# Kernel optimization log

Hardware: AMD Instinct MI355X
Metric: run time of the kernel (lower is better)

Reference implementation:

```python
import jax, jax.numpy as jnp
import numpy as np

TEMPERATURE = 0.07
ALPHA = 1.0
GAMMA = 2.0
EPS = 1e-12  # F.normalize eps


def _l2_normalize(x):
    # matches F.normalize: x / max(||x||_2, eps)
    norm = jnp.sqrt(jnp.sum(x * x, axis=-1, keepdims=True))
    return x / jnp.maximum(norm, EPS)


def setup_inputs() -> dict:
    key = jax.random.key(0)
    k1, k2 = jax.random.split(key)
    B, D = 8192, 64
    image_features = jax.random.normal(k1, (B, D), dtype=jnp.float32)
    text_features = jax.random.normal(k2, (B, D), dtype=jnp.float32)
    return {"image_features": image_features, "text_features": text_features}


def reference(image_features, text_features):
    img = _l2_normalize(image_features)
    txt = _l2_normalize(text_features)
    logits = jnp.einsum("bd,cd->bc", img, txt) / TEMPERATURE  # [B, B]
    B = logits.shape[0]
    idx = jnp.arange(B)

    logp_row = jax.nn.log_softmax(logits, axis=-1)  # i2t CE source
    logp_col = jax.nn.log_softmax(logits, axis=0)   # t2i CE source

    diag_logp_row = logp_row[idx, idx]
    diag_logp_col = logp_col[idx, idx]

    # focal weight uses ROW-softmax positive prob for BOTH directions (as in source)
    p_pos = jnp.exp(diag_logp_row)
    w = ALPHA * (1.0 - p_pos) ** GAMMA

    focal_i2t = jnp.mean(w * (-diag_logp_row))
    focal_t2i = jnp.mean(w * (-diag_logp_col))
    return (focal_i2t + focal_t2i) / 2.0
```

## Files before the change

kernel.cpp:

```cpp
#include <hip/hip_runtime.h>
#include <hip/hip_bf16.h>


#define NB 8192
#define ND 64

constexpr float INV_T = 1.0f / 0.07f;
constexpr float LOG2E = 1.4426950408889634f;
constexpr float LN2   = 0.6931471805599453f;
constexpr float K1    = INV_T * LOG2E;

typedef float  floatx4 __attribute__((ext_vector_type(4)));
typedef short  bf16x8  __attribute__((ext_vector_type(8)));
typedef short  shortx4 __attribute__((ext_vector_type(4)));

__global__ __launch_bounds__(256)
void norm_kernel(const float* __restrict__ img, const float* __restrict__ txt,
                 __hip_bfloat16* __restrict__ imgB,
                 __hip_bfloat16* __restrict__ txtB,
                 float* __restrict__ diag,
                 float* __restrict__ rowSum,
                 float* __restrict__ colSum,
                 float* __restrict__ out)
{
    const int tid = blockIdx.x * 256 + threadIdx.x;
    if (tid < NB) { rowSum[tid] = 0.f; colSum[tid] = 0.f; }
    if (tid == 0) out[0] = 0.f;

    const int lane = threadIdx.x & 63;
    const int gw   = blockIdx.x * 4 + (threadIdx.x >> 6);
    const int sub  = lane >> 4;
    const int c16  = lane & 15;
    const int row  = gw * 4 + sub;

    const floatx4 x = ((const floatx4*)img)[row * 16 + c16];
    const floatx4 t = ((const floatx4*)txt)[row * 16 + c16];
    float sx  = x[0]*x[0] + x[1]*x[1] + x[2]*x[2] + x[3]*x[3];
    float st  = t[0]*t[0] + t[1]*t[1] + t[2]*t[2] + t[3]*t[3];
    float sxt = x[0]*t[0] + x[1]*t[1] + x[2]*t[2] + x[3]*t[3];
    #pragma unroll
    for (int o = 1; o < 16; o <<= 1) {
        sx  += __shfl_xor(sx,  o, 64);
        st  += __shfl_xor(st,  o, 64);
        sxt += __shfl_xor(sxt, o, 64);
    }
    const float nx = fmaxf(sqrtf(sx), 1e-12f);
    const float nt = fmaxf(sqrtf(st), 1e-12f);
    shortx4 xb, tb;
    #pragma unroll
    for (int j = 0; j < 4; ++j) {
        __hip_bfloat16 hx = __float2bfloat16(x[j] / nx * K1);
        __hip_bfloat16 ht = __float2bfloat16(t[j] / nt);
        xb[j] = *reinterpret_cast<const short*>(&hx);
        tb[j] = *reinterpret_cast<const short*>(&ht);
    }
    ((shortx4*)imgB)[row * 16 + c16] = xb;
    ((shortx4*)txtB)[row * 16 + c16] = tb;
    if (c16 == 0) diag[row] = sxt / (nx * nt) * INV_T;
}

__global__ __launch_bounds__(256)
void score_kernel(const __hip_bfloat16* __restrict__ imgB,
                  const __hip_bfloat16* __restrict__ txtB,
                  float* __restrict__ rowSum,
                  float* __restrict__ colSum)
{
    const int wid   = threadIdx.x >> 6;
    const int lane  = threadIdx.x & 63;
    const int gw    = blockIdx.x * 4 + wid;
    const int strip = gw >> 5;
    const int chunk = gw & 31;
    const int m = lane & 15;
    const int q = lane >> 4;

    const bf16x8* __restrict__ A  = (const bf16x8*)imgB;
    const bf16x8* __restrict__ Bp = (const bf16x8*)txtB;

    const int rowbase = strip * 64;
    bf16x8 a[4][2];
    #pragma unroll
    for (int it = 0; it < 4; ++it) {
        const int r = rowbase + it * 16 + m;
        a[it][0] = A[r * 8 + q];
        a[it][1] = A[r * 8 + 4 + q];
    }

    const int colbase = chunk * 256 + m;
    bf16x8 b0 = Bp[colbase * 8 + q];
    bf16x8 b1 = Bp[colbase * 8 + 4 + q];

    float rs[16];
    #pragma unroll
    for (int i = 0; i < 16; ++i) rs[i] = 0.f;

    const floatx4 NEGK = {-K1, -K1, -K1, -K1};

    #pragma unroll 2
    for (int t = 0; t < 16; ++t) {
        const int nn = colbase + (((t + 1) & 15) << 4);
        const bf16x8 pb0 = Bp[nn * 8 + q];
        const bf16x8 pb1 = Bp[nn * 8 + 4 + q];

        float csp[4];
        #pragma unroll
        for (int it = 0; it < 4; ++it) {
            floatx4 z   = __builtin_amdgcn_mfma_f32_16x16x32_bf16(a[it][0], b0, NEGK, 0, 0, 0);
            floatx4 acc = __builtin_amdgcn_mfma_f32_16x16x32_bf16(a[it][1], b1, z,    0, 0, 0);
            const float e0 = __builtin_amdgcn_exp2f(acc[0]);
            const float e1 = __builtin_amdgcn_exp2f(acc[1]);
            const float e2 = __builtin_amdgcn_exp2f(acc[2]);
            const float e3 = __builtin_amdgcn_exp2f(acc[3]);
            rs[it * 4 + 0] += e0;
            rs[it * 4 + 1] += e1;
            rs[it * 4 + 2] += e2;
            rs[it * 4 + 3] += e3;
            csp[it] = (e0 + e1) + (e2 + e3);
        }
        float cs = (csp[0] + csp[1]) + (csp[2] + csp[3]);
        cs += __shfl_xor(cs, 16, 64);
        cs += __shfl_xor(cs, 32, 64);
        if (q == 0)
            unsafeAtomicAdd(&colSum[colbase + (t << 4)], cs);
        b0 = pb0; b1 = pb1;
    }

#define RS_STAGE(d)                                                     \
    {                                                                   \
        const bool hi = (m & (d)) != 0;                                 \
        _Pragma("unroll")                                               \
        for (int j = 0; j < (d); ++j) {                                 \
            const float va = rs[j], vb = rs[j + (d)];                   \
            const float send = hi ? va : vb;                            \
            const float recv = __shfl_xor(send, (d), 64);               \
            rs[j] = (hi ? vb : va) + recv;                              \
        }                                                               \
    }
    RS_STAGE(8)
    RS_STAGE(4)
    RS_STAGE(2)
    RS_STAGE(1)
#undef RS_STAGE

    const int row = rowbase + ((m >> 2) << 4) + (q << 2) + (m & 3);
    unsafeAtomicAdd(&rowSum[row], rs[0]);
}

__global__ __launch_bounds__(256)
void finish_kernel(const float* __restrict__ rowSum,
                   const float* __restrict__ colSum,
                   const float* __restrict__ diag,
                   float* __restrict__ out)
{
    const int i = blockIdx.x * 256 + threadIdx.x;
    const float rowS = rowSum[i];
    const float colS = colSum[i];
    const float d     = diag[i];
    const float lse_r = INV_T + __builtin_amdgcn_logf(rowS) * LN2;
    const float lse_c = INV_T + __builtin_amdgcn_logf(colS) * LN2;
    const float lpr = d - lse_r;
    const float lpc = d - lse_c;
    const float p   = __builtin_amdgcn_exp2f(lpr * LOG2E);
    const float om  = 1.f - p;
    float contrib = om * om * (-lpr - lpc) * (0.5f / (float)NB);

    #pragma unroll
    for (int o = 1; o < 64; o <<= 1) contrib += __shfl_xor(contrib, o, 64);
    __shared__ float red[4];
    if ((threadIdx.x & 63) == 0) red[threadIdx.x >> 6] = contrib;
    __syncthreads();
    if (threadIdx.x == 0)
        atomicAdd(out, red[0] + red[1] + red[2] + red[3]);
}

extern "C" void kernel_launch(void* const* d_in, const int* in_sizes, int n_in,
                              void* d_out, int out_size, void* d_ws, size_t ws_size,
                              hipStream_t stream)
{
    const float* img = (const float*)d_in[0];
    const float* txt = (const float*)d_in[1];

    char* ws = (char*)d_ws;
    __hip_bfloat16* imgB = (__hip_bfloat16*)(ws);
    __hip_bfloat16* txtB = (__hip_bfloat16*)(ws + (1u << 20));
    float* diag   = (float*)(ws + (2u << 20));
    float* rowSum = (float*)(ws + (2u << 20) + (1u << 15));
    float* colSum = (float*)(ws + (2u << 20) + (2u << 15));

    norm_kernel<<<512, 256, 0, stream>>>(img, txt, imgB, txtB, diag, rowSum, colSum, (float*)d_out);
    score_kernel<<<1024, 256, 0, stream>>>(imgB, txtB, rowSum, colSum);
    finish_kernel<<<NB / 256, 256, 0, stream>>>(rowSum, colSum, diag, (float*)d_out);
}
```

Before: 83.15 us.

## Replace global atomics with per-chunk partial sums reduced in finish kernel

Column sums are now combined across the four waves of a block in shared memory, and each block writes its row and column partials to separate workspace slots. This replaces the per-tile global atomic adds. Block indexing is remapped so the four waves of a block share one column chunk. The finish kernel now reduces the 32 partials per index with 8 lanes per index, and the zeroing of the sum buffers in norm_kernel is dropped. The cost is extra workspace traffic (about 2 MB of partials) and a heavier finish kernel.

```diff
diff --git a/kernel.cpp b/kernel.cpp
--- a/kernel.cpp
+++ b/kernel.cpp
@@ -19,13 +19,9 @@
                  __hip_bfloat16* __restrict__ imgB,
                  __hip_bfloat16* __restrict__ txtB,
                  float* __restrict__ diag,
-                 float* __restrict__ rowSum,
-                 float* __restrict__ colSum,
                  float* __restrict__ out)
 {
-    const int tid = blockIdx.x * 256 + threadIdx.x;
-    if (tid < NB) { rowSum[tid] = 0.f; colSum[tid] = 0.f; }
-    if (tid == 0) out[0] = 0.f;
+    if (blockIdx.x == 0 && threadIdx.x == 0) out[0] = 0.f;
 
     const int lane = threadIdx.x & 63;
     const int gw   = blockIdx.x * 4 + (threadIdx.x >> 6);
@@ -62,16 +58,18 @@
 __global__ __launch_bounds__(256)
 void score_kernel(const __hip_bfloat16* __restrict__ imgB,
                   const __hip_bfloat16* __restrict__ txtB,
-                  float* __restrict__ rowSum,
-                  float* __restrict__ colSum)
+                  float* __restrict__ rowPart,
+                  float* __restrict__ colPart)
 {
     const int wid   = threadIdx.x >> 6;
     const int lane  = threadIdx.x & 63;
-    const int gw    = blockIdx.x * 4 + wid;
-    const int strip = gw >> 5;
-    const int chunk = gw & 31;
+    const int chunk = blockIdx.x & 31;
+    const int sgrp  = blockIdx.x >> 5;
+    const int strip = sgrp * 4 + wid;
     const int m = lane & 15;
     const int q = lane >> 4;
+
+    __shared__ float sm[4][256];
 
     const bf16x8* __restrict__ A  = (const bf16x8*)imgB;
     const bf16x8* __restrict__ Bp = (const bf16x8*)txtB;
@@ -119,8 +117,7 @@
         float cs = (csp[0] + csp[1]) + (csp[2] + csp[3]);
         cs += __shfl_xor(cs, 16, 64);
         cs += __shfl_xor(cs, 32, 64);
-        if (q == 0)
-            unsafeAtomicAdd(&colSum[colbase + (t << 4)], cs);
+        if (q == 0) sm[wid][(t << 4) + m] = cs;
         b0 = pb0; b1 = pb1;
     }
 
@@ -142,29 +139,50 @@
 #undef RS_STAGE
 
     const int row = rowbase + ((m >> 2) << 4) + (q << 2) + (m & 3);
-    unsafeAtomicAdd(&rowSum[row], rs[0]);
+    rowPart[chunk * NB + row] = rs[0];
+
+    __syncthreads();
+    const int j = threadIdx.x;
+    const float v = (sm[0][j] + sm[1][j]) + (sm[2][j] + sm[3][j]);
+    colPart[sgrp * NB + chunk * 256 + j] = v;
 }
 
 __global__ __launch_bounds__(256)
-void finish_kernel(const float* __restrict__ rowSum,
-                   const float* __restrict__ colSum,
+void finish_kernel(const float* __restrict__ rowPart,
+                   const float* __restrict__ colPart,
                    const float* __restrict__ diag,
                    float* __restrict__ out)
 {
-    const int i = blockIdx.x * 256 + threadIdx.x;
-    const float rowS = rowSum[i];
-    const float colS = colSum[i];
-    const float d     = diag[i];
-    const float lse_r = INV_T + __builtin_amdgcn_logf(rowS) * LN2;
-    const float lse_c = INV_T + __builtin_amdgcn_logf(colS) * LN2;
-    const float lpr = d - lse_r;
-    const float lpc = d - lse_c;
-    const float p   = __builtin_amdgcn_exp2f(lpr * LOG2E);
-    const float om  = 1.f - p;
-    float contrib = om * om * (-lpr - lpc) * (0.5f / (float)NB);
-
-    #pragma unroll
-    for (int o = 1; o < 64; o <<= 1) contrib += __shfl_xor(contrib, o, 64);
+    const int tg = blockIdx.x * 256 + threadIdx.x;
+    const int i  = tg >> 3;
+    const int p  = threadIdx.x & 7;
+
+    float rowS = 0.f, colS = 0.f;
+    #pragma unroll
+    for (int u = 0; u < 4; ++u) {
+        rowS += rowPart[(p * 4 + u) * NB + i];
+        colS += colPart[(p * 4 + u) * NB + i];
+    }
+    #pragma unroll
+    for (int o = 1; o < 8; o <<= 1) {
+        rowS += __shfl_xor(rowS, o, 64);
+        colS += __shfl_xor(colS, o, 64);
+    }
+
+    float contrib = 0.f;
+    if (p == 0) {
+        const float d     = diag[i];
+        const float lse_r = INV_T + __builtin_amdgcn_logf(rowS) * LN2;
+        const float lse_c = INV_T + __builtin_amdgcn_logf(colS) * LN2;
+        const float lpr = d - lse_r;
+        const float lpc = d - lse_c;
+        const float pp  = __builtin_amdgcn_exp2f(lpr * LOG2E);
+        const float om  = 1.f - pp;
+        contrib = om * om * (-lpr - lpc) * (0.5f / (float)NB);
+    }
+    #pragma unroll
+    for (int o = 8; o < 64; o <<= 1) contrib += __shfl_xor(contrib, o, 64);
+
     __shared__ float red[4];
     if ((threadIdx.x & 63) == 0) red[threadIdx.x >> 6] = contrib;
     __syncthreads();
@@ -182,11 +200,11 @@
     char* ws = (char*)d_ws;
     __hip_bfloat16* imgB = (__hip_bfloat16*)(ws);
     __hip_bfloat16* txtB = (__hip_bfloat16*)(ws + (1u << 20));
-    float* diag   = (float*)(ws + (2u << 20));
-    float* rowSum = (float*)(ws + (2u << 20) + (1u << 15));
-    float* colSum = (float*)(ws + (2u << 20) + (2u << 15));
-
-    norm_kernel<<<512, 256, 0, stream>>>(img, txt, imgB, txtB, diag, rowSum, colSum, (float*)d_out);
-    score_kernel<<<1024, 256, 0, stream>>>(imgB, txtB, rowSum, colSum);
-    finish_kernel<<<NB / 256, 256, 0, stream>>>(rowSum, colSum, diag, (float*)d_out);
-}
+    float* diag    = (float*)(ws + (2u << 20));
+    float* rowPart = (float*)(ws + (2u << 20) + (1u << 15));
+    float* colPart = (float*)(ws + (3u << 20) + (1u << 15));
+
+    norm_kernel<<<512, 256, 0, stream>>>(img, txt, imgB, txtB, diag, (float*)d_out);
+    score_kernel<<<1024, 256, 0, stream>>>(imgB, txtB, rowPart, colPart);
+    finish_kernel<<<256, 256, 0, stream>>>(rowPart, colPart, diag, (float*)d_out);
+}
```

After: 84.71 us. About the same (+1.9%).
